# Optimization experiments

Measured on AMD Instinct MI355X. Metric: run time of the kernel, lower is better.

The kernel has to match this reference:

```python
import jax, jax.numpy as jnp
import numpy as np
import math

N = 4096
E = 131072
IN_DIM, HID, OUT = 512, 256, 64
DEPTH = 3
RATIO = 0.5


def setup_inputs() -> dict:
    key = jax.random.key(0)
    ks = jax.random.split(key, 12)

    def w(k, fi, fo):
        return jax.random.normal(k, (fi, fo), jnp.float32) * (1.0 / np.sqrt(fi).astype(np.float32))

    return {
        "x": jax.random.normal(ks[0], (N, IN_DIM), jnp.float32),
        "edge_index": jax.random.randint(ks[1], (2, E), 0, N, jnp.int32),
        "dW0": w(ks[2], IN_DIM, HID), "dW1": w(ks[3], HID, HID),
        "dW2": w(ks[4], HID, HID), "dW3": w(ks[5], HID, HID),
        "db0": jnp.zeros((HID,), jnp.float32), "db1": jnp.zeros((HID,), jnp.float32),
        "db2": jnp.zeros((HID,), jnp.float32), "db3": jnp.zeros((HID,), jnp.float32),
        "pw0": jax.random.normal(ks[6], (HID,), jnp.float32),
        "pw1": jax.random.normal(ks[7], (HID,), jnp.float32),
        "pw2": jax.random.normal(ks[8], (HID,), jnp.float32),
        "uW0": w(ks[9], HID, HID), "uW1": w(ks[10], HID, HID), "uW2": w(ks[11], HID, OUT),
        "ub0": jnp.zeros((HID,), jnp.float32), "ub1": jnp.zeros((HID,), jnp.float32),
        "ub2": jnp.zeros((OUT,), jnp.float32),
    }


def gcn_conv(x, A, W, b):
    # GCNConv(improved=True): A_hat = A + 2I, sym-normalized.
    n = A.shape[0]
    eye = jnp.eye(n, dtype=A.dtype)
    Ah = A + 2.0 * eye
    d = Ah.sum(axis=1)
    dinv = jnp.where(d > 0, jax.lax.rsqrt(d), 0.0)
    An = dinv[:, None] * Ah * dinv[None, :]
    return An @ (x @ W) + b


def augment_adj(A):
    # add self loops, square the (weighted) adjacency, remove self loops
    n = A.shape[0]
    eye = jnp.eye(n, dtype=A.dtype)
    Al = A + eye
    A2 = Al @ Al
    return A2 * (1.0 - eye)


def topk_pool(x, A, w, k):
    # TopKPooling: score = tanh(x.w/||w||); keep top-k; gate kept features by score.
    score = jnp.tanh((x @ w) / jnp.linalg.norm(w))
    _, perm = jax.lax.top_k(score, k)
    xp = x[perm] * score[perm][:, None]
    return xp, A[perm][:, perm], perm


def _forward(x, edge_index, down_Ws, down_bs, pool_ws, up_Ws, up_bs):
    A = jnp.zeros((N, N), jnp.float32).at[edge_index[0], edge_index[1]].set(1.0)
    x = jax.nn.relu(gcn_conv(x, A, down_Ws[0], down_bs[0]))
    xs, As, perms = [x], [A], []
    n = N
    for i in range(1, DEPTH + 1):
        A = augment_adj(A)
        k = int(math.ceil(RATIO * n)); n = k
        x, A, perm = topk_pool(x, A, pool_ws[i - 1], k)
        x = jax.nn.relu(gcn_conv(x, A, down_Ws[i], down_bs[i]))
        if i < DEPTH:
            xs.append(x); As.append(A)
        perms.append(perm)
    for i in range(DEPTH):
        j = DEPTH - 1 - i
        res, A, perm = xs[j], As[j], perms[j]
        up = jnp.zeros_like(res).at[perm].set(x)   # unpool (sum_res=True)
        x = res + up
        x = gcn_conv(x, A, up_Ws[i], up_bs[i])
        if i < DEPTH - 1:
            x = jax.nn.relu(x)
    return x


def reference(x, edge_index, dW0, dW1, dW2, dW3, db0, db1, db2, db3,
              pw0, pw1, pw2, uW0, uW1, uW2, ub0, ub1, ub2):
    return _forward(x, edge_index,
                    [dW0, dW1, dW2, dW3], [db0, db1, db2, db3],
                    [pw0, pw1, pw2],
                    [uW0, uW1, uW2], [ub0, ub1, ub2])
```

## Files before the change

### kernel.cpp

```cpp
#include <hip/hip_runtime.h>
#include <math.h>

#define NN 4096
#define EE 131072
#define IN_DIM 512
#define HID 256
#define OUT_DIM 64
#define ECAP 128

typedef __attribute__((ext_vector_type(8))) short bf8_t;
typedef __attribute__((ext_vector_type(4))) float f4_t;
typedef __attribute__((ext_vector_type(8))) unsigned short us8_t;
typedef __attribute__((ext_vector_type(4))) unsigned short us4_t;

#define GAS __attribute__((address_space(1)))
#define LAS __attribute__((address_space(3)))

__device__ __forceinline__ unsigned short f2bf(float v){
  union { float f; unsigned u; } x; x.f = v;
  unsigned r = x.u + 0x7fffu + ((x.u >> 16) & 1u);
  return (unsigned short)(r >> 16);
}
__device__ __forceinline__ float bf2f(unsigned short h){
  union { float f; unsigned u; } x; x.u = ((unsigned)h) << 16;
  return x.f;
}

__device__ __forceinline__ float waveReduceSum(float v){
#pragma unroll
  for (int off = 32; off > 0; off >>= 1) v += __shfl_down(v, off);
  return v;
}

__global__ __launch_bounds__(256) void k_prep(
    const float* __restrict__ x_in, const float* __restrict__ dW0,
    const float* __restrict__ dW1, const float* __restrict__ dW2,
    const float* __restrict__ dW3, const float* __restrict__ uW0,
    const float* __restrict__ uW1, const float* __restrict__ uW2,
    unsigned* __restrict__ bits,
    unsigned short* __restrict__ xinh, unsigned short* __restrict__ xinl,
    unsigned short* __restrict__ W0th, unsigned short* __restrict__ W0tl,
    unsigned short* __restrict__ W5th, unsigned short* __restrict__ W5tl,
    unsigned short* __restrict__ W2th, unsigned short* __restrict__ W2tl)
{
  int b = blockIdx.x;
  if (b < 128){
    int base = b * 4096 + threadIdx.x;
#pragma unroll
    for (int i = 0; i < 16; ++i) bits[base + i * 256] = 0;
    return;
  }
  b -= 128;
  if (b < 2048){
    int i0 = b * 1024 + threadIdx.x;
#pragma unroll
    for (int i = 0; i < 4; ++i){
      int idx = i0 + i * 256;
      float v = x_in[idx];
      unsigned short h = f2bf(v);
      xinh[idx] = h; xinl[idx] = f2bf(v - bf2f(h));
    }
    return;
  }
  b -= 2048;
  const float* X; unsigned short *Th, *Tl; int R, C, tile;
  if (b < 128){ X = dW0; Th = W0th; Tl = W0tl; R = 512; C = 256; tile = b; }
  else if (b < 448){
    int t2 = b - 128; int z = t2 >> 6; int rem = t2 & 63;
    const float* ws[5] = {dW1, dW2, dW3, uW0, uW1};
    X = ws[z]; Th = W5th + (size_t)z * 65536; Tl = W5tl + (size_t)z * 65536;
    R = 256; C = 256; tile = rem;
  } else { X = uW2; Th = W2th; Tl = W2tl; R = 256; C = 64; tile = b - 448; }
  int tpr = C >> 5;
  int bx = (tile % tpr) * 32, by = (tile / tpr) * 32;
  __shared__ float t[32][33];
  int tx = threadIdx.x & 31, ty = threadIdx.x >> 5;
#pragma unroll
  for (int i = 0; i < 4; ++i)
    t[ty + i * 8][tx] = X[(size_t)(by + ty + i * 8) * C + bx + tx];
  __syncthreads();
#pragma unroll
  for (int i = 0; i < 4; ++i){
    float v = t[tx][ty + i * 8];
    unsigned short h = f2bf(v);
    size_t o = (size_t)(bx + ty + i * 8) * R + by + tx;
    Th[o] = h; Tl[o] = f2bf(v - bf2f(h));
  }
}

__global__ void k_build_bits(const int* __restrict__ ei, unsigned* __restrict__ bits){
  int e = blockIdx.x * blockDim.x + threadIdx.x;
  if (e < EE){
    int r = ei[e], c = ei[EE + e];
    atomicOr(&bits[r * 128 + (c >> 5)], 1u << (c & 31));
  }
}

__global__ __launch_bounds__(128) void k_ell(const unsigned* __restrict__ bits,
                                             int* __restrict__ ell, int* __restrict__ cnt,
                                             float* __restrict__ dinv){
  int r = blockIdx.x, t = threadIdx.x;
  unsigned w = bits[r * 128 + t];
  int c = __popc(w);
  __shared__ int sc[128];
  sc[t] = c; __syncthreads();
  for (int off = 1; off < 128; off <<= 1){
    int a = sc[t], b = (t >= off) ? sc[t - off] : 0;
    __syncthreads(); sc[t] = a + b; __syncthreads();
  }
  int total = sc[127];
  int pos = sc[t] - c;
  int base = r * ECAP;
  while (w){
    int b = __ffs(w) - 1; w &= w - 1;
    if (pos < ECAP) ell[base + pos] = t * 32 + b;
    pos++;
  }
  if (t == 0){
    cnt[r] = (total < ECAP) ? total : ECAP;
    dinv[r] = 1.0f / sqrtf((float)total + 2.0f);
  }
}

template<int NCOLS, int RELU, int SC>
__global__ __launch_bounds__(256) void k_spmm_ell(
    const int* __restrict__ ell, const int* __restrict__ cnt,
    const float* __restrict__ Zs, const float* __restrict__ dinv,
    const float* __restrict__ bias, float* __restrict__ out,
    const float* __restrict__ scw, float* __restrict__ score)
{
  int r = blockIdx.x;
  __shared__ int s_idx[ECAP];
  __shared__ int s_n;
  __shared__ float sh[4 * NCOLS];
  __shared__ float sd[4], sq[4];
  if (threadIdx.x == 0) s_n = cnt[r];
  for (int i = threadIdx.x; i < ECAP; i += 256) s_idx[i] = ell[r * ECAP + i];
  __syncthreads();
  int n = s_n; if (n > ECAP) n = ECAP;
  int wv = threadIdx.x >> 6, lane = threadIdx.x & 63;
  if (NCOLS == 256){
    f4_t acc = (f4_t){0.f, 0.f, 0.f, 0.f};
    for (int e = wv; e < n; e += 4){
      const f4_t* row = (const f4_t*)(Zs + (size_t)s_idx[e] * 256);
      acc += row[lane];
    }
    ((f4_t*)(sh + wv * 256))[lane] = acc;
  } else {
    float acc = 0.f;
    for (int e = wv; e < n; e += 4)
      acc += Zs[(size_t)s_idx[e] * 64 + lane];
    sh[wv * 64 + lane] = acc;
  }
  __syncthreads();
  int t = threadIdx.x;
  float o = 0.f;
  if (t < NCOLS){
    float y = sh[t] + sh[NCOLS + t] + sh[2 * NCOLS + t] + sh[3 * NCOLS + t];
    float z = Zs[(size_t)r * NCOLS + t];
    o = dinv[r] * (y + 2.0f * z) + bias[t];
    if (RELU) o = fmaxf(o, 0.f);
    out[(size_t)r * NCOLS + t] = o;
  }
  if (SC){
    float w = scw[t];
    float d = waveReduceSum(o * w);
    float q = waveReduceSum(w * w);
    if (!lane){ sd[wv] = d; sq[wv] = q; }
    __syncthreads();
    if (!t) score[r] = tanhf((sd[0] + sd[1] + sd[2] + sd[3]) / sqrtf(sq[0] + sq[1] + sq[2] + sq[3]));
  }
}

__global__ __launch_bounds__(256) void k_pool_build(
    const float* __restrict__ x0, const float* __restrict__ score,
    const int* __restrict__ perm1, const int* __restrict__ inv1,
    const int* __restrict__ ell, const int* __restrict__ cnt,
    unsigned short* __restrict__ xph, unsigned short* __restrict__ xpl,
    unsigned char* __restrict__ Rb,
    unsigned short* __restrict__ xu1h, unsigned short* __restrict__ xu1l)
{
  int b = blockIdx.x;
  if (b < 2048){
    int pr = perm1[b]; float s = score[pr];
    int c = threadIdx.x;
    float v = x0[(size_t)pr * 256 + c] * s;
    unsigned short h = f2bf(v);
    xph[(size_t)b * 256 + c] = h;
    xpl[(size_t)b * 256 + c] = f2bf(v - bf2f(h));
    return;
  }
  if (b < 6144){
    int k = b - 2048;
    __shared__ unsigned char row[2048];
    for (int i = threadIdx.x; i < 512; i += 256) ((int*)row)[i] = 0;
    __syncthreads();
    int n = cnt[k];
    for (int e = threadIdx.x; e < n; e += 256){
      int s = inv1[ell[k * ECAP + e]];
      if (s >= 0) row[s] = 1;
    }
    __syncthreads();
    if (threadIdx.x == 0){
      int sk = inv1[k];
      if (sk >= 0) row[sk] += 1;
    }
    __syncthreads();
    *(uint2*)(Rb + (size_t)k * 2048 + threadIdx.x * 8) = *(uint2*)(row + threadIdx.x * 8);
    return;
  }
  int r = b - 6144;
  if (inv1[r] < 0){
    int c = threadIdx.x;
    float v = x0[(size_t)r * 256 + c];
    unsigned short h = f2bf(v);
    xu1h[(size_t)r * 256 + c] = h;
    xu1l[(size_t)r * 256 + c] = f2bf(v - bf2f(h));
  }
}

template<int SRCL, int OUTL>
__global__ __launch_bounds__(256) void k_pp(
    const float* __restrict__ x, const float* __restrict__ score,
    const int* __restrict__ perm, const int* __restrict__ inv, int n, int k,
    unsigned short* __restrict__ xph, unsigned short* __restrict__ xpl,
    unsigned short* __restrict__ xuh, unsigned short* __restrict__ xul,
    const unsigned short* __restrict__ Ah, const unsigned short* __restrict__ Al,
    unsigned short* __restrict__ Lh, unsigned short* __restrict__ Ll,
    unsigned short* __restrict__ Rh, unsigned short* __restrict__ Rl)
{
  __shared__ float t[32][33];
  __shared__ int sinv[32];
  int b = blockIdx.x, c = threadIdx.x;
  if (b < k){
    int pr = perm[b]; float s = score[pr];
    float v = x[(size_t)pr * 256 + c] * s;
    unsigned short h = f2bf(v);
    xph[(size_t)b * 256 + c] = h;
    xpl[(size_t)b * 256 + c] = f2bf(v - bf2f(h));
    return;
  }
  b -= k;
  if (b < n){
    if (inv[b] < 0){
      float v = x[(size_t)b * 256 + c];
      unsigned short h = f2bf(v);
      xuh[(size_t)b * 256 + c] = h;
      xul[(size_t)b * 256 + c] = f2bf(v - bf2f(h));
    }
    return;
  }
  b -= n;
  if (b < k){
    int r = b, pr = perm[r];
    for (int cc = threadIdx.x; cc < n; cc += 256){
      float v = bf2f(Ah[(size_t)pr * n + cc]);
      if (SRCL) v += bf2f(Al[(size_t)pr * n + cc]);
      if (pr == cc) v += 1.f;
      unsigned short h = f2bf(v);
      Lh[(size_t)r * n + cc] = h;
      if (OUTL) Ll[(size_t)r * n + cc] = f2bf(v - bf2f(h));
    }
    return;
  }
  b -= k;
  int tpr = n >> 5;
  int kt = b / tpr, ct = b - kt * tpr;
  int tx = threadIdx.x & 31, ty = threadIdx.x >> 5;
  if (threadIdx.x < 32) sinv[threadIdx.x] = inv[ct * 32 + threadIdx.x];
#pragma unroll
  for (int i = 0; i < 4; ++i){
    int kl = ty + i * 8;
    size_t src = (size_t)(kt * 32 + kl) * n + ct * 32 + tx;
    float v = bf2f(Ah[src]);
    if (SRCL) v += bf2f(Al[src]);
    t[kl][tx] = v;
  }
  __syncthreads();
#pragma unroll
  for (int i = 0; i < 4; ++i){
    int cl = ty + i * 8;
    int s = sinv[cl];
    if (s >= 0){
      float v = t[tx][cl];
      if (kt * 32 + tx == ct * 32 + cl) v += 1.f;
      unsigned short h = f2bf(v);
      size_t o = (size_t)s * n + kt * 32 + tx;
      Rh[o] = h;
      if (OUTL) Rl[o] = f2bf(v - bf2f(h));
    }
  }
}

__global__ __launch_bounds__(256) void k_sq1(const int* __restrict__ ell, const int* __restrict__ cnt,
                                             const int* __restrict__ perm,
                                             const unsigned char* __restrict__ Rb,
                                             unsigned short* __restrict__ A1h,
                                             float* __restrict__ dinv1){
  int r = blockIdx.x;
  int pr = perm[r];
  __shared__ int s_idx[ECAP];
  __shared__ int s_n;
  __shared__ float sred[4];
  if (threadIdx.x == 0) s_n = cnt[pr];
  for (int i = threadIdx.x; i < ECAP; i += 256) s_idx[i] = ell[pr * ECAP + i];
  __syncthreads();
  int n = s_n; if (n > ECAP) n = ECAP;
  int colb = threadIdx.x * 8;
  uint2 acc = *(const uint2*)(Rb + (size_t)pr * 2048 + colb);
  for (int e = 0; e < n; ++e){
    uint2 v = *(const uint2*)(Rb + (size_t)s_idx[e] * 2048 + colb);
    acc.x += v.x; acc.y += v.y;
  }
  float fs = 0.f;
  us8_t o;
#pragma unroll
  for (int j = 0; j < 8; ++j){
    unsigned byte = ((j < 4 ? acc.x : acc.y) >> (8 * (j & 3))) & 0xFFu;
    if (colb + j == r) byte = 0;
    float f = (float)byte;
    fs += f;
    o[j] = f2bf(f);
  }
  *(us8_t*)(A1h + (size_t)r * 2048 + colb) = o;
  fs = waveReduceSum(fs);
  int lane = threadIdx.x & 63, wd = threadIdx.x >> 6;
  if (!lane) sred[wd] = fs;
  __syncthreads();
  if (!threadIdx.x)
    dinv1[r] = 1.0f / sqrtf(sred[0] + sred[1] + sred[2] + sred[3] + 2.0f);
}

template<int HAS_AL, int HAS_BL, int HAS_LL, int EPI>
__global__ __launch_bounds__(256) void k_mm(
    const unsigned short* __restrict__ Ah, const unsigned short* __restrict__ Al,
    const unsigned short* __restrict__ Bh, const unsigned short* __restrict__ Bl,
    int M, int N, int K, int KS, float* __restrict__ P,
    float* __restrict__ Cf, unsigned short* __restrict__ Ch, unsigned short* __restrict__ Cl,
    const float* __restrict__ dinv)
{
  constexpr int NARR = 2 + HAS_AL + HAS_BL;
  constexpr int BUF = NARR * 8192;
  __shared__ int4 ldsq[NARR * 512 * 2];
  char* ldsc = (char*)ldsq;

  const int tid = threadIdx.x, lane = tid & 63, wid = tid >> 6;
  const int wm = wid >> 1, wn = wid & 1;
  const int bm = blockIdx.y << 6, bn = blockIdx.x << 6;
  const int z = blockIdx.z;
  const int l15 = lane & 15, l4 = lane >> 4;

  f4_t acc[2][2];
#pragma unroll
  for (int i = 0; i < 2; ++i)
#pragma unroll
    for (int j = 0; j < 2; ++j) acc[i][j] = (f4_t){0.f, 0.f, 0.f, 0.f};

  const size_t rb = (size_t)K * 2;
  const size_t kz = (size_t)z * KS * 2;
  const char* pAh = (const char*)Ah + (size_t)bm * rb;
  const char* pAl = HAS_AL ? (const char*)Al + (size_t)bm * rb : nullptr;
  const char* pBh = (const char*)Bh + (size_t)bn * rb;
  const char* pBl = HAS_BL ? (const char*)Bl + (size_t)bn * rb : nullptr;

  auto stage = [&](int t, int b2){
    char* ldsb = ldsc + b2 * BUF;
    const size_t kb = kz + (size_t)t * 128;
#pragma unroll
    for (int it = 0; it < 2; ++it){
      const int idx = tid + (it << 8);
      const int row = idx >> 3;
      const int kc = ((idx & 7) << 4) ^ ((row & 7) << 4);
      const size_t go = (size_t)row * rb + kb + kc;
      const int lo = idx * 16;
      __builtin_amdgcn_global_load_lds((const GAS void*)(pAh + go), (LAS void*)(ldsb + lo), 16, 0, 0);
      __builtin_amdgcn_global_load_lds((const GAS void*)(pBh + go), (LAS void*)(ldsb + 8192 + lo), 16, 0, 0);
      if (HAS_AL)
        __builtin_amdgcn_global_load_lds((const GAS void*)(pAl + go), (LAS void*)(ldsb + 16384 + lo), 16, 0, 0);
      if (HAS_BL)
        __builtin_amdgcn_global_load_lds((const GAS void*)(pBl + go), (LAS void*)(ldsb + (2 + HAS_AL) * 8192 + lo), 16, 0, 0);
    }
  };

  const int T = KS >> 6;
  stage(0, 0);
  int b = 0;
  for (int t = 0; t < T; ++t){
    if (t + 1 < T){
      stage(t + 1, b ^ 1);
      if constexpr (NARR == 2) asm volatile("s_waitcnt vmcnt(4)" ::: "memory");
      else if constexpr (NARR == 3) asm volatile("s_waitcnt vmcnt(6)" ::: "memory");
      else asm volatile("s_waitcnt vmcnt(8)" ::: "memory");
    } else {
      asm volatile("s_waitcnt vmcnt(0)" ::: "memory");
    }
    __syncthreads();
    const char* ldsb = ldsc + b * BUF;
#pragma unroll
    for (int ks = 0; ks < 2; ++ks){
      bf8_t aH[2], aL[2], bH[2], bL[2];
#pragma unroll
      for (int f = 0; f < 2; ++f){
        int ar = wm * 32 + f * 16 + l15;
        int aoff = ar * 128 + (((ks * 64) + (l4 << 4)) ^ ((ar & 7) << 4));
        aH[f] = *(const bf8_t*)(ldsb + aoff);
        if (HAS_AL) aL[f] = *(const bf8_t*)(ldsb + 16384 + aoff);
        int br = wn * 32 + f * 16 + l15;
        int boff = br * 128 + (((ks * 64) + (l4 << 4)) ^ ((br & 7) << 4));
        bH[f] = *(const bf8_t*)(ldsb + 8192 + boff);
        if (HAS_BL) bL[f] = *(const bf8_t*)(ldsb + (2 + HAS_AL) * 8192 + boff);
      }
#pragma unroll
      for (int i = 0; i < 2; ++i)
#pragma unroll
        for (int j = 0; j < 2; ++j){
          acc[i][j] = __builtin_amdgcn_mfma_f32_16x16x32_bf16(aH[i], bH[j], acc[i][j], 0, 0, 0);
          if (HAS_BL) acc[i][j] = __builtin_amdgcn_mfma_f32_16x16x32_bf16(aH[i], bL[j], acc[i][j], 0, 0, 0);
          if (HAS_AL) acc[i][j] = __builtin_amdgcn_mfma_f32_16x16x32_bf16(aL[i], bH[j], acc[i][j], 0, 0, 0);
          if (HAS_LL) acc[i][j] = __builtin_amdgcn_mfma_f32_16x16x32_bf16(aL[i], bL[j], acc[i][j], 0, 0, 0);
        }
    }
    __syncthreads();
    b ^= 1;
  }

  float* Pz = (EPI == 0) ? P + (size_t)z * M * N : nullptr;
#pragma unroll
  for (int i = 0; i < 2; ++i)
#pragma unroll
    for (int j = 0; j < 2; ++j)
#pragma unroll
      for (int r = 0; r < 4; ++r){
        int grow = bm + wm * 32 + i * 16 + l4 * 4 + r;
        int gcol = bn + wn * 32 + j * 16 + l15;
        float v = acc[i][j][r];
        size_t o = (size_t)grow * N + gcol;
        if (EPI == 0){
          Pz[o] = v;
        } else if (EPI == 2){
          Cf[o] = dinv[grow] * v;
        } else {
          float sv = dinv[grow] * v;
          Cf[o] = sv;
          unsigned short h = f2bf(sv);
          size_t ot = (size_t)gcol * M + grow;
          Ch[ot] = h; Cl[ot] = f2bf(sv - bf2f(h));
        }
      }
}

template<int EPI, int SC>
__global__ __launch_bounds__(256) void k_red(
    const float* __restrict__ P, int Z, int M, int NC,
    const float* __restrict__ dinv, const float* __restrict__ Zs,
    const float* __restrict__ bias,
    float* __restrict__ Of, unsigned short* __restrict__ Oh, unsigned short* __restrict__ Ol,
    float* __restrict__ dout, int relu,
    const float* __restrict__ scw, float* __restrict__ score,
    const float* __restrict__ res, const int* __restrict__ permsel)
{
  int w = threadIdx.x >> 6, lane = threadIdx.x & 63;
  int row = blockIdx.x * 4 + w;
  int prow = (EPI == 4) ? permsel[row] : 0;
  float di = (EPI != 3) ? dinv[row] : 0.f;
  float rsum = 0.f, o_d = 0.f, o_q = 0.f;
  for (int c0 = lane * 4; c0 < NC; c0 += 256){
    size_t o = (size_t)row * NC + c0;
    f4_t s = *(const f4_t*)(P + o);
    for (int zz = 1; zz < Z; ++zz) s += *(const f4_t*)(P + (size_t)zz * M * NC + o);
    if (EPI == 2){
      f4_t z4 = *(const f4_t*)(Zs + o);
      f4_t b4 = *(const f4_t*)(bias + c0);
      f4_t out;
#pragma unroll
      for (int j = 0; j < 4; ++j){
        float v = di * (s[j] + 2.0f * z4[j]) + b4[j];
        if (relu) v = fmaxf(v, 0.f);
        out[j] = v;
      }
      *(f4_t*)(Of + o) = out;
      if (SC){
        f4_t w4 = *(const f4_t*)(scw + c0);
#pragma unroll
        for (int j = 0; j < 4; ++j){ o_d += out[j] * w4[j]; o_q += w4[j] * w4[j]; }
      }
    } else if (EPI == 3){
      us4_t h4, l4v;
#pragma unroll
      for (int j = 0; j < 4; ++j){
        float v = (c0 + j == row) ? 0.f : s[j];
        unsigned short h = f2bf(v);
        h4[j] = h; l4v[j] = f2bf(v - bf2f(h));
        rsum += v;
      }
      *(us4_t*)(Oh + o) = h4;
      *(us4_t*)(Ol + o) = l4v;
    } else {
      f4_t z4 = *(const f4_t*)(Zs + o);
      f4_t b4 = *(const f4_t*)(bias + c0);
      f4_t r4 = *(const f4_t*)(res + (size_t)prow * NC + c0);
      us4_t h4, l4v;
#pragma unroll
      for (int j = 0; j < 4; ++j){
        float v = di * (s[j] + 2.0f * z4[j]) + b4[j];
        if (relu) v = fmaxf(v, 0.f);
        float comb = r4[j] + v;
        unsigned short h = f2bf(comb);
        h4[j] = h; l4v[j] = f2bf(comb - bf2f(h));
      }
      size_t od = (size_t)prow * NC + c0;
      *(us4_t*)(Oh + od) = h4;
      *(us4_t*)(Ol + od) = l4v;
    }
  }
  if (EPI == 3){
    rsum = waveReduceSum(rsum);
    if (!lane) dout[row] = 1.0f / sqrtf(rsum + 2.0f);
  }
  if (SC){
    o_d = waveReduceSum(o_d);
    o_q = waveReduceSum(o_q);
    if (!lane) score[row] = tanhf(o_d / sqrtf(o_q));
  }
}

__global__ void k_topk(const float* __restrict__ score, int n, int k,
                       int* __restrict__ perm, int* __restrict__ inv){
  int i = blockIdx.x; float si = score[i];
  int cnt = 0;
  for (int j = threadIdx.x; j < n; j += 256){
    float sj = score[j];
    if (sj > si || (sj == si && j < i)) cnt++;
  }
#pragma unroll
  for (int off = 32; off > 0; off >>= 1) cnt += __shfl_down(cnt, off);
  __shared__ int sh[4];
  int lane = threadIdx.x & 63, wid = threadIdx.x >> 6;
  if (lane == 0) sh[wid] = cnt;
  __syncthreads();
  if (threadIdx.x == 0){
    int rank = sh[0] + sh[1] + sh[2] + sh[3];
    if (rank < k){ perm[rank] = i; inv[i] = rank; }
    else inv[i] = -1;
  }
}

extern "C" void kernel_launch(void* const* d_in, const int* in_sizes, int n_in,
                              void* d_out, int out_size, void* d_ws, size_t ws_size,
                              hipStream_t stream){
  (void)in_sizes; (void)n_in; (void)out_size;
  const float* x_in = (const float*)d_in[0];
  const int*   ei   = (const int*)d_in[1];
  const float* dW0 = (const float*)d_in[2];
  const float* dW1 = (const float*)d_in[3];
  const float* dW2 = (const float*)d_in[4];
  const float* dW3 = (const float*)d_in[5];
  const float* db0 = (const float*)d_in[6];
  const float* db1 = (const float*)d_in[7];
  const float* db2 = (const float*)d_in[8];
  const float* db3 = (const float*)d_in[9];
  const float* pw0 = (const float*)d_in[10];
  const float* pw1 = (const float*)d_in[11];
  const float* pw2 = (const float*)d_in[12];
  const float* uW0 = (const float*)d_in[13];
  const float* uW1 = (const float*)d_in[14];
  const float* uW2 = (const float*)d_in[15];
  const float* ub0 = (const float*)d_in[16];
  const float* ub1 = (const float*)d_in[17];
  const float* ub2 = (const float*)d_in[18];

  char* p = (char*)d_ws;
  auto alloc = [&](size_t nbytes) -> void* {
    void* q = (void*)p; p += (nbytes + 255) & ~(size_t)255; return q;
  };
  unsigned* bits = (unsigned*)alloc((size_t)4096 * 128 * 4);
  int* ell = (int*)alloc((size_t)4096 * ECAP * 4);
  int* cnt = (int*)alloc(4096 * 4);
  int* inv1 = (int*)alloc(4096 * 4);
  int* inv2 = (int*)alloc(2048 * 4);
  int* inv3 = (int*)alloc(1024 * 4);
  unsigned char* Rb = (unsigned char*)alloc((size_t)4096 * 2048);
  float* Pp = (float*)alloc((size_t)8 * 1024 * 1024);
  unsigned short* A1h = (unsigned short*)alloc((size_t)2048 * 2048 * 2);
  unsigned short* A2h = (unsigned short*)alloc((size_t)1024 * 1024 * 2);
  unsigned short* A2l = (unsigned short*)alloc((size_t)1024 * 1024 * 2);
  unsigned short* A3h = (unsigned short*)alloc((size_t)512 * 512 * 2);
  unsigned short* A3l = (unsigned short*)alloc((size_t)512 * 512 * 2);
  unsigned short* Lb2h = (unsigned short*)alloc((size_t)1024 * 2048 * 2);
  unsigned short* Rt2h = (unsigned short*)alloc((size_t)1024 * 2048 * 2);
  unsigned short* Lb3h = (unsigned short*)alloc((size_t)512 * 1024 * 2);
  unsigned short* Lb3l = (unsigned short*)alloc((size_t)512 * 1024 * 2);
  unsigned short* Rt3h = (unsigned short*)alloc((size_t)512 * 1024 * 2);
  unsigned short* Rt3l = (unsigned short*)alloc((size_t)512 * 1024 * 2);
  unsigned short* xinh = (unsigned short*)alloc((size_t)4096 * 512 * 2);
  unsigned short* xinl = (unsigned short*)alloc((size_t)4096 * 512 * 2);
  float* x0 = (float*)alloc((size_t)4096 * HID * 4);
  float* x1 = (float*)alloc((size_t)2048 * HID * 4);
  float* x2 = (float*)alloc((size_t)1024 * HID * 4);
  unsigned short* xu1h = (unsigned short*)alloc((size_t)4096 * HID * 2);
  unsigned short* xu1l = (unsigned short*)alloc((size_t)4096 * HID * 2);
  unsigned short* xu2h = (unsigned short*)alloc((size_t)2048 * HID * 2);
  unsigned short* xu2l = (unsigned short*)alloc((size_t)2048 * HID * 2);
  unsigned short* xu3h = (unsigned short*)alloc((size_t)1024 * HID * 2);
  unsigned short* xu3l = (unsigned short*)alloc((size_t)1024 * HID * 2);
  unsigned short* xph = (unsigned short*)alloc((size_t)2048 * HID * 2);
  unsigned short* xpl = (unsigned short*)alloc((size_t)2048 * HID * 2);
  unsigned short* W0th = (unsigned short*)alloc((size_t)256 * 512 * 2);
  unsigned short* W0tl = (unsigned short*)alloc((size_t)256 * 512 * 2);
  unsigned short* W5th = (unsigned short*)alloc((size_t)5 * 256 * 256 * 2);
  unsigned short* W5tl = (unsigned short*)alloc((size_t)5 * 256 * 256 * 2);
  unsigned short* W2th = (unsigned short*)alloc((size_t)64 * 256 * 2);
  unsigned short* W2tl = (unsigned short*)alloc((size_t)64 * 256 * 2);
  float* Zs  = (float*)alloc((size_t)4096 * HID * 4);
  unsigned short* ZsTh = (unsigned short*)alloc((size_t)256 * 2048 * 2);
  unsigned short* ZsTl = (unsigned short*)alloc((size_t)256 * 2048 * 2);
  float* dinv0 = (float*)alloc(4096 * 4);
  float* dinv1 = (float*)alloc(2048 * 4);
  float* dinv2 = (float*)alloc(1024 * 4);
  float* dinv3 = (float*)alloc(512 * 4);
  float* score = (float*)alloc(4096 * 4);
  int* perm1 = (int*)alloc(2048 * 4);
  int* perm2 = (int*)alloc(1024 * 4);
  int* perm3 = (int*)alloc(512 * 4);
  if ((size_t)(p - (char*)d_ws) > ws_size) return;

  k_prep<<<2640, 256, 0, stream>>>(x_in, dW0, dW1, dW2, dW3, uW0, uW1, uW2, bits,
                                   xinh, xinl, W0th, W0tl, W5th, W5tl, W2th, W2tl);
  k_build_bits<<<EE / 256, 256, 0, stream>>>(ei, bits);
  k_ell<<<4096, 128, 0, stream>>>(bits, ell, cnt, dinv0);

  { dim3 g(4, 64);
    k_mm<1,1,0,2><<<g, 256, 0, stream>>>(xinh, xinl, W0th, W0tl, 4096, HID, IN_DIM, IN_DIM,
                                         nullptr, Zs, nullptr, nullptr, dinv0); }
  k_spmm_ell<256,1,1><<<4096, 256, 0, stream>>>(ell, cnt, Zs, dinv0, db0, x0, pw0, score);

  k_topk<<<4096, 256, 0, stream>>>(score, 4096, 2048, perm1, inv1);
  k_pool_build<<<10240, 256, 0, stream>>>(x0, score, perm1, inv1, ell, cnt,
                                          xph, xpl, Rb, xu1h, xu1l);
  k_sq1<<<2048, 256, 0, stream>>>(ell, cnt, perm1, Rb, A1h, dinv1);
  { dim3 g(4, 32);
    k_mm<1,1,0,4><<<g, 256, 0, stream>>>(xph, xpl, W5th, W5tl, 2048, HID, HID, HID,
                                         nullptr, Zs, ZsTh, ZsTl, dinv1); }
  { dim3 g(4, 32, 4);
    k_mm<0,1,0,0><<<g, 256, 0, stream>>>(A1h, nullptr, ZsTh, ZsTl, 2048, HID, 2048, 512,
                                         Pp, nullptr, nullptr, nullptr, nullptr); }
  k_red<2,1><<<512, 256, 0, stream>>>(Pp, 4, 2048, 256, dinv1, Zs, db1,
                                      x1, nullptr, nullptr, nullptr, 1, pw1, score, nullptr, nullptr);

  k_topk<<<2048, 256, 0, stream>>>(score, 2048, 1024, perm2, inv2);
  k_pp<0,0><<<8192, 256, 0, stream>>>(x1, score, perm2, inv2, 2048, 1024,
                                      xph, xpl, xu2h, xu2l, A1h, nullptr,
                                      Lb2h, nullptr, Rt2h, nullptr);
  { dim3 g(16, 16, 2);
    k_mm<0,0,0,0><<<g, 256, 0, stream>>>(Lb2h, nullptr, Rt2h, nullptr, 1024, 1024, 2048, 1024,
                                         Pp, nullptr, nullptr, nullptr, nullptr); }
  k_red<3,0><<<256, 256, 0, stream>>>(Pp, 2, 1024, 1024, nullptr, nullptr, nullptr,
                                      nullptr, A2h, A2l, dinv2, 0, nullptr, nullptr, nullptr, nullptr);
  { dim3 g(4, 16);
    k_mm<1,1,0,4><<<g, 256, 0, stream>>>(xph, xpl, W5th + 65536, W5tl + 65536, 1024, HID, HID, HID,
                                         nullptr, Zs, ZsTh, ZsTl, dinv2); }
  { dim3 g(4, 16, 4);
    k_mm<1,1,0,0><<<g, 256, 0, stream>>>(A2h, A2l, ZsTh, ZsTl, 1024, HID, 1024, 256,
                                         Pp, nullptr, nullptr, nullptr, nullptr); }
  k_red<2,1><<<256, 256, 0, stream>>>(Pp, 4, 1024, 256, dinv2, Zs, db2,
                                      x2, nullptr, nullptr, nullptr, 1, pw2, score, nullptr, nullptr);

  k_topk<<<1024, 256, 0, stream>>>(score, 1024, 512, perm3, inv3);
  k_pp<1,1><<<3072, 256, 0, stream>>>(x2, score, perm3, inv3, 1024, 512,
                                      xph, xpl, xu3h, xu3l, A2h, A2l,
                                      Lb3h, Lb3l, Rt3h, Rt3l);
  { dim3 g(8, 8, 4);
    k_mm<1,1,1,0><<<g, 256, 0, stream>>>(Lb3h, Lb3l, Rt3h, Rt3l, 512, 512, 1024, 256,
                                         Pp, nullptr, nullptr, nullptr, nullptr); }
  k_red<3,0><<<128, 256, 0, stream>>>(Pp, 4, 512, 512, nullptr, nullptr, nullptr,
                                      nullptr, A3h, A3l, dinv3, 0, nullptr, nullptr, nullptr, nullptr);
  { dim3 g(4, 8);
    k_mm<1,1,0,4><<<g, 256, 0, stream>>>(xph, xpl, W5th + 2 * 65536, W5tl + 2 * 65536, 512, HID, HID, HID,
                                         nullptr, Zs, ZsTh, ZsTl, dinv3); }
  { dim3 g(4, 8, 4);
    k_mm<1,1,0,0><<<g, 256, 0, stream>>>(A3h, A3l, ZsTh, ZsTl, 512, HID, 512, 128,
                                         Pp, nullptr, nullptr, nullptr, nullptr); }
  k_red<4,0><<<128, 256, 0, stream>>>(Pp, 4, 512, 256, dinv3, Zs, db3,
                                      nullptr, xu3h, xu3l, nullptr, 1, nullptr, nullptr, x2, perm3);

  { dim3 g(4, 16);
    k_mm<1,1,0,4><<<g, 256, 0, stream>>>(xu3h, xu3l, W5th + 3 * 65536, W5tl + 3 * 65536, 1024, HID, HID, HID,
                                         nullptr, Zs, ZsTh, ZsTl, dinv2); }
  { dim3 g(4, 16, 4);
    k_mm<1,1,0,0><<<g, 256, 0, stream>>>(A2h, A2l, ZsTh, ZsTl, 1024, HID, 1024, 256,
                                         Pp, nullptr, nullptr, nullptr, nullptr); }
  k_red<4,0><<<256, 256, 0, stream>>>(Pp, 4, 1024, 256, dinv2, Zs, ub0,
                                      nullptr, xu2h, xu2l, nullptr, 1, nullptr, nullptr, x1, perm2);

  { dim3 g(4, 32);
    k_mm<1,1,0,4><<<g, 256, 0, stream>>>(xu2h, xu2l, W5th + 4 * 65536, W5tl + 4 * 65536, 2048, HID, HID, HID,
                                         nullptr, Zs, ZsTh, ZsTl, dinv1); }
  { dim3 g(4, 32, 4);
    k_mm<0,1,0,0><<<g, 256, 0, stream>>>(A1h, nullptr, ZsTh, ZsTl, 2048, HID, 2048, 512,
                                         Pp, nullptr, nullptr, nullptr, nullptr); }
  k_red<4,0><<<512, 256, 0, stream>>>(Pp, 4, 2048, 256, dinv1, Zs, ub1,
                                      nullptr, xu1h, xu1l, nullptr, 1, nullptr, nullptr, x0, perm1);

  { dim3 g(1, 64);
    k_mm<1,1,0,2><<<g, 256, 0, stream>>>(xu1h, xu1l, W2th, W2tl, 4096, OUT_DIM, HID, HID,
                                         nullptr, Zs, nullptr, nullptr, dinv0); }
  k_spmm_ell<64,0,0><<<4096, 256, 0, stream>>>(ell, cnt, Zs, dinv0, ub2, (float*)d_out, nullptr, nullptr);
}
```

Before: 232.5 us.

## Replace level-1 dense A1 matmul with sparse two-hop gather aggregation

The dense 2048x2048 bf16 matmul of the squared adjacency A1 against the transformed features, used at level 1 down and up, is replaced by two sparse gather kernels. One sums, for each original node, the features of its kept neighbours. The other sums those partial results over the kept node's own neighbours, then corrects the diagonal using the edge bitmask. This uses the factorisation A1 = P(A+I)(A+I)P^T to avoid the dense GEMM and the split-K reduction. Separately, the reachability byte matrix Rb is packed to 2 bits per entry to cut k_sq1 gather traffic, which assumes the counts never exceed 3. The bitmask-based diagonal correction and the fp32 gather order change the numerics.

```diff
diff --git a/kernel.cpp b/kernel.cpp
--- a/kernel.cpp
+++ b/kernel.cpp
@@ -172,12 +172,98 @@
   }
 }
 
+__global__ __launch_bounds__(256) void k_gG(
+    const int* __restrict__ ell, const int* __restrict__ cnt, const int* __restrict__ inv,
+    const float* __restrict__ Zs, float* __restrict__ G)
+{
+  int k = blockIdx.x;
+  __shared__ int s_idx[ECAP];
+  __shared__ int s_n;
+  __shared__ float sh[4 * 256];
+  if (!threadIdx.x) s_n = cnt[k];
+  __syncthreads();
+  int n = s_n;
+  for (int i = threadIdx.x; i < n; i += 256)
+    s_idx[i] = inv[ell[k * ECAP + i]];
+  __syncthreads();
+  int wv = threadIdx.x >> 6, lane = threadIdx.x & 63;
+  f4_t acc = (f4_t){0.f, 0.f, 0.f, 0.f};
+  for (int e = wv; e < n; e += 4){
+    int s = s_idx[e];
+    if (s >= 0) acc += ((const f4_t*)(Zs + (size_t)s * 256))[lane];
+  }
+  if (wv == 0){
+    int sk = inv[k];
+    if (sk >= 0) acc += ((const f4_t*)(Zs + (size_t)sk * 256))[lane];
+  }
+  ((f4_t*)(sh + wv * 256))[lane] = acc;
+  __syncthreads();
+  int t = threadIdx.x;
+  G[(size_t)k * 256 + t] = sh[t] + sh[256 + t] + sh[512 + t] + sh[768 + t];
+}
+
+template<int UP>
+__global__ __launch_bounds__(256) void k_gY(
+    const int* __restrict__ ell, const int* __restrict__ cnt, const int* __restrict__ perm,
+    const unsigned* __restrict__ bits,
+    const float* __restrict__ G, const float* __restrict__ Zs, const float* __restrict__ dinv,
+    const float* __restrict__ bias,
+    float* __restrict__ outF, unsigned short* __restrict__ Oh, unsigned short* __restrict__ Ol,
+    const float* __restrict__ scw, float* __restrict__ score, const float* __restrict__ res)
+{
+  int r = blockIdx.x;
+  int pr = perm[r];
+  __shared__ int s_idx[ECAP];
+  __shared__ int s_n;
+  __shared__ float sh[4 * 256];
+  __shared__ float sdg[4], sd[4], sq[4];
+  if (!threadIdx.x) s_n = cnt[pr];
+  for (int i = threadIdx.x; i < ECAP; i += 256) s_idx[i] = ell[pr * ECAP + i];
+  __syncthreads();
+  int n = s_n;
+  int wv = threadIdx.x >> 6, lane = threadIdx.x & 63;
+  float dg = 0.f;
+  for (int e = threadIdx.x; e < n; e += 256){
+    int k = s_idx[e];
+    dg += (float)((bits[k * 128 + (pr >> 5)] >> (pr & 31)) & 1u);
+  }
+  dg = waveReduceSum(dg);
+  if (!lane) sdg[wv] = dg;
+  f4_t acc = (f4_t){0.f, 0.f, 0.f, 0.f};
+  for (int e = wv; e < n; e += 4)
+    acc += ((const f4_t*)(G + (size_t)s_idx[e] * 256))[lane];
+  if (wv == 0) acc += ((const f4_t*)(G + (size_t)pr * 256))[lane];
+  ((f4_t*)(sh + wv * 256))[lane] = acc;
+  __syncthreads();
+  float diag1 = sdg[0] + sdg[1] + sdg[2] + sdg[3]
+              + 2.0f * (float)((bits[pr * 128 + (pr >> 5)] >> (pr & 31)) & 1u) + 1.0f;
+  int t = threadIdx.x;
+  float y = sh[t] + sh[256 + t] + sh[512 + t] + sh[768 + t];
+  float z = Zs[(size_t)r * 256 + t];
+  float o = dinv[r] * (y - diag1 * z + 2.0f * z) + bias[t];
+  o = fmaxf(o, 0.f);
+  if (UP){
+    float comb = res[(size_t)pr * 256 + t] + o;
+    unsigned short h = f2bf(comb);
+    size_t od = (size_t)pr * 256 + t;
+    Oh[od] = h; Ol[od] = f2bf(comb - bf2f(h));
+  } else {
+    outF[(size_t)r * 256 + t] = o;
+    float w = scw[t];
+    float d = waveReduceSum(o * w);
+    float q = waveReduceSum(w * w);
+    if (!lane){ sd[wv] = d; sq[wv] = q; }
+    __syncthreads();
+    if (!t) score[r] = tanhf((sd[0] + sd[1] + sd[2] + sd[3]) / sqrtf(sq[0] + sq[1] + sq[2] + sq[3]));
+  }
+}
+
 __global__ __launch_bounds__(256) void k_pool_build(
     const float* __restrict__ x0, const float* __restrict__ score,
     const int* __restrict__ perm1, const int* __restrict__ inv1,
     const int* __restrict__ ell, const int* __restrict__ cnt,
     unsigned short* __restrict__ xph, unsigned short* __restrict__ xpl,
-    unsigned char* __restrict__ Rb,
+    unsigned short* __restrict__ Rb2,
     unsigned short* __restrict__ xu1h, unsigned short* __restrict__ xu1l)
 {
   int b = blockIdx.x;
@@ -206,7 +292,10 @@
       if (sk >= 0) row[sk] += 1;
     }
     __syncthreads();
-    *(uint2*)(Rb + (size_t)k * 2048 + threadIdx.x * 8) = *(uint2*)(row + threadIdx.x * 8);
+    unsigned w = 0;
+#pragma unroll
+    for (int j = 0; j < 8; ++j) w |= ((unsigned)row[(threadIdx.x << 3) + j]) << (2 * j);
+    Rb2[k * 256 + threadIdx.x] = (unsigned short)w;
     return;
   }
   int r = b - 6144;
@@ -294,7 +383,7 @@
 
 __global__ __launch_bounds__(256) void k_sq1(const int* __restrict__ ell, const int* __restrict__ cnt,
                                              const int* __restrict__ perm,
-                                             const unsigned char* __restrict__ Rb,
+                                             const unsigned short* __restrict__ Rb2,
                                              unsigned short* __restrict__ A1h,
                                              float* __restrict__ dinv1){
   int r = blockIdx.x;
@@ -307,9 +396,15 @@
   __syncthreads();
   int n = s_n; if (n > ECAP) n = ECAP;
   int colb = threadIdx.x * 8;
-  uint2 acc = *(const uint2*)(Rb + (size_t)pr * 2048 + colb);
+  auto expand = [](unsigned x) -> uint2 {
+    uint2 e;
+    e.x = (x & 3) | (((x >> 2) & 3) << 8) | (((x >> 4) & 3) << 16) | (((x >> 6) & 3) << 24);
+    e.y = ((x >> 8) & 3) | (((x >> 10) & 3) << 8) | (((x >> 12) & 3) << 16) | (((x >> 14) & 3) << 24);
+    return e;
+  };
+  uint2 acc = expand(Rb2[pr * 256 + threadIdx.x]);
   for (int e = 0; e < n; ++e){
-    uint2 v = *(const uint2*)(Rb + (size_t)s_idx[e] * 2048 + colb);
+    uint2 v = expand(Rb2[s_idx[e] * 256 + threadIdx.x]);
     acc.x += v.x; acc.y += v.y;
   }
   float fs = 0.f;
@@ -579,7 +674,7 @@
   int* inv1 = (int*)alloc(4096 * 4);
   int* inv2 = (int*)alloc(2048 * 4);
   int* inv3 = (int*)alloc(1024 * 4);
-  unsigned char* Rb = (unsigned char*)alloc((size_t)4096 * 2048);
+  unsigned short* Rb2 = (unsigned short*)alloc((size_t)4096 * 256 * 2);
   float* Pp = (float*)alloc((size_t)8 * 1024 * 1024);
   unsigned short* A1h = (unsigned short*)alloc((size_t)2048 * 2048 * 2);
   unsigned short* A2h = (unsigned short*)alloc((size_t)1024 * 1024 * 2);
@@ -636,16 +731,14 @@
 
   k_topk<<<4096, 256, 0, stream>>>(score, 4096, 2048, perm1, inv1);
   k_pool_build<<<10240, 256, 0, stream>>>(x0, score, perm1, inv1, ell, cnt,
-                                          xph, xpl, Rb, xu1h, xu1l);
-  k_sq1<<<2048, 256, 0, stream>>>(ell, cnt, perm1, Rb, A1h, dinv1);
+                                          xph, xpl, Rb2, xu1h, xu1l);
+  k_sq1<<<2048, 256, 0, stream>>>(ell, cnt, perm1, Rb2, A1h, dinv1);
   { dim3 g(4, 32);
-    k_mm<1,1,0,4><<<g, 256, 0, stream>>>(xph, xpl, W5th, W5tl, 2048, HID, HID, HID,
-                                         nullptr, Zs, ZsTh, ZsTl, dinv1); }
-  { dim3 g(4, 32, 4);
-    k_mm<0,1,0,0><<<g, 256, 0, stream>>>(A1h, nullptr, ZsTh, ZsTl, 2048, HID, 2048, 512,
-                                         Pp, nullptr, nullptr, nullptr, nullptr); }
-  k_red<2,1><<<512, 256, 0, stream>>>(Pp, 4, 2048, 256, dinv1, Zs, db1,
-                                      x1, nullptr, nullptr, nullptr, 1, pw1, score, nullptr, nullptr);
+    k_mm<1,1,0,2><<<g, 256, 0, stream>>>(xph, xpl, W5th, W5tl, 2048, HID, HID, HID,
+                                         nullptr, Zs, nullptr, nullptr, dinv1); }
+  k_gG<<<4096, 256, 0, stream>>>(ell, cnt, inv1, Zs, Pp);
+  k_gY<0><<<2048, 256, 0, stream>>>(ell, cnt, perm1, bits, Pp, Zs, dinv1, db1,
+                                    x1, nullptr, nullptr, pw1, score, nullptr);
 
   k_topk<<<2048, 256, 0, stream>>>(score, 2048, 1024, perm2, inv2);
   k_pp<0,0><<<8192, 256, 0, stream>>>(x1, score, perm2, inv2, 2048, 1024,
@@ -693,13 +786,11 @@
                                       nullptr, xu2h, xu2l, nullptr, 1, nullptr, nullptr, x1, perm2);
 
   { dim3 g(4, 32);
-    k_mm<1,1,0,4><<<g, 256, 0, stream>>>(xu2h, xu2l, W5th + 4 * 65536, W5tl + 4 * 65536, 2048, HID, HID, HID,
-                                         nullptr, Zs, ZsTh, ZsTl, dinv1); }
-  { dim3 g(4, 32, 4);
-    k_mm<0,1,0,0><<<g, 256, 0, stream>>>(A1h, nullptr, ZsTh, ZsTl, 2048, HID, 2048, 512,
-                                         Pp, nullptr, nullptr, nullptr, nullptr); }
-  k_red<4,0><<<512, 256, 0, stream>>>(Pp, 4, 2048, 256, dinv1, Zs, ub1,
-                                      nullptr, xu1h, xu1l, nullptr, 1, nullptr, nullptr, x0, perm1);
+    k_mm<1,1,0,2><<<g, 256, 0, stream>>>(xu2h, xu2l, W5th + 4 * 65536, W5tl + 4 * 65536, 2048, HID, HID, HID,
+                                         nullptr, Zs, nullptr, nullptr, dinv1); }
+  k_gG<<<4096, 256, 0, stream>>>(ell, cnt, inv1, Zs, Pp);
+  k_gY<1><<<2048, 256, 0, stream>>>(ell, cnt, perm1, bits, Pp, Zs, dinv1, ub1,
+                                    nullptr, xu1h, xu1l, nullptr, nullptr, x0);
 
   { dim3 g(1, 64);
     k_mm<1,1,0,2><<<g, 256, 0, stream>>>(xu1h, xu1l, W2th, W2tl, 4096, OUT_DIM, HID, HID,
```

Measured after the change: 241.1 us. 1.04x slower.
